# Performance work log

Hardware: AMD Instinct MI355X
Metric: run time of the kernel (lower is better)

The kernel has to match this reference:

```python
import jax, jax.numpy as jnp
import numpy as np

B, C, D, H, W = 8, 256, 128, 64, 64  # batch, in_channels, inter_dim, spatial
BN_EPS = 1e-5


def setup_inputs() -> dict:
    key = jax.random.key(0)
    ks = jax.random.split(key, 6)
    s_c = 1.0 / np.sqrt(C)
    s_d = 1.0 / np.sqrt(D)
    return {
        "x": jax.random.normal(ks[0], (B, C, H, W), dtype=jnp.float32),
        # 1x1 conv kernels, stored as [out_ch, in_ch]
        "theta_w": jax.random.normal(ks[1], (D, C), dtype=jnp.float32) * s_c,
        "phi_w": jax.random.normal(ks[2], (D, C), dtype=jnp.float32) * s_c,
        "g_w": jax.random.normal(ks[3], (D, C), dtype=jnp.float32) * s_c,
        "w_w": jax.random.normal(ks[4], (C, D), dtype=jnp.float32) * s_d,
        "w_b": jnp.zeros((C,), dtype=jnp.float32),
        "bn_gamma": jnp.ones((C,), dtype=jnp.float32),
        "bn_beta": jnp.zeros((C,), dtype=jnp.float32),
    }


def reference(x, theta_w, phi_w, g_w, w_w, w_b, bn_gamma, bn_beta):
    Bs, Cs, Hs, Ws = x.shape
    N = Hs * Ws
    xf = x.reshape(Bs, Cs, N)  # flatten spatial -> [B, C, N]

    # 1x1 convs (bias=False) == per-position channel matmuls
    theta = jnp.einsum('dc,bcn->bnd', theta_w, xf)  # [B, N, D]
    phi = jnp.einsum('dc,bcn->bdn', phi_w, xf)      # [B, D, N]
    g = jnp.einsum('dc,bcn->bnd', g_w, xf)          # [B, N, D]

    # embedded-Gaussian attention: softmax(theta @ phi) @ g
    f = jnp.einsum('bnd,bdm->bnm', theta, phi)      # [B, N, N]
    f_div_C = jax.nn.softmax(f, axis=-1)
    y = jnp.einsum('bnm,bmd->bnd', f_div_C, g)      # [B, N, D]

    # output projection W (1x1 conv with bias)
    w_y = jnp.einsum('cd,bnd->bcn', w_w, y) + w_b[None, :, None]  # [B, C, N]

    # BatchNorm (training mode: batch statistics, biased variance)
    mean = w_y.mean(axis=(0, 2))
    var = jnp.mean(jnp.square(w_y - mean[None, :, None]), axis=(0, 2))
    scale = (bn_gamma * jax.lax.rsqrt(var + BN_EPS))[None, :, None]
    w_y = (w_y - mean[None, :, None]) * scale + bn_beta[None, :, None]

    z = w_y + xf  # residual
    return z.reshape(Bs, Cs, Hs, Ws)
```

## Files before the change

### kernel.cpp

```cpp
#include <hip/hip_runtime.h>

#define BB 8
#define CC 256
#define DD 128
#define NN 4096
#define BN_EPS 1e-5f

typedef _Float16 f16;
typedef _Float16 half8 __attribute__((ext_vector_type(8)));
typedef _Float16 half2t __attribute__((ext_vector_type(2)));
typedef float f32x4 __attribute__((ext_vector_type(4)));

__device__ __forceinline__ f32x4 mfma16(half8 a, half8 b, f32x4 c) {
  return __builtin_amdgcn_mfma_f32_16x16x32_f16(a, b, c, 0, 0, 0);
}

__device__ __forceinline__ void gload_lds16(const void* g, void* l) {
  __builtin_amdgcn_global_load_lds((const __attribute__((address_space(1))) void*)g,
                                   (__attribute__((address_space(3))) void*)l, 16, 0, 0);
}

__device__ __forceinline__ half2t pkrtz(float a, float b) {
  auto t = __builtin_amdgcn_cvt_pkrtz(a, b);
  return __builtin_bit_cast(half2t, t);
}

#define EXP2(x) __builtin_amdgcn_exp2f(x)

#define PERM32(i) ((((i) >> 2) & 3) * 8 + (((i) >> 4) & 1) * 4 + ((i) & 3))

__global__ void k_cast_weights(const float* __restrict__ tw, const float* __restrict__ pw,
                               const float* __restrict__ gw, const float* __restrict__ ww,
                               f16* __restrict__ Wcat, f16* __restrict__ Wwh,
                               float* __restrict__ stats) {
  int i = blockIdx.x * 256 + threadIdx.x;
  if (i < 32768) Wcat[i] = (f16)tw[i];
  else if (i < 65536) Wcat[i] = (f16)pw[i - 32768];
  else if (i < 98304) Wcat[i] = (f16)gw[i - 65536];
  else if (i < 131072) Wwh[i - 98304] = (f16)ww[i - 98304];
  if (i < 512) stats[i] = 0.f;
}

__global__ __launch_bounds__(256) void k_gemm1(const float* __restrict__ x, const f16* __restrict__ Wcat,
                                               f16* __restrict__ T, f16* __restrict__ P,
                                               f16* __restrict__ Gdn) {
  __shared__ char xls[32768];
  __shared__ char gls[16384];
  int b = blockIdx.y;
  int n0 = blockIdx.x * 64;
  int tid = threadIdx.x;
  int lane = tid & 63, wave = tid >> 6;
  int lr = lane & 15, lg = lane >> 4;
  int wr = wave >> 1, wc = wave & 1;

  {
    int c = tid;
    const float* src = x + ((size_t)b * CC + c) * NN + n0;
#pragma unroll
    for (int n4 = 0; n4 < 64; n4 += 4) {
      f32x4 v = *(const f32x4*)(src + n4);
#pragma unroll
      for (int k = 0; k < 4; ++k) {
        int n = n4 + k;
        *(f16*)(xls + n * 512 + ((((c >> 3) ^ (n & 7)) * 8 + (c & 7)) * 2)) = (f16)v[k];
      }
    }
  }
  __syncthreads();

  half8 a[2][8];
#pragma unroll
  for (int i = 0; i < 2; ++i) {
    int nloc = wr * 32 + i * 16 + lr;
#pragma unroll
    for (int k0 = 0; k0 < 8; ++k0)
      a[i][k0] = *(const half8*)(xls + nloc * 512 + (((k0 * 4 + lg) ^ (nloc & 7)) << 4));
  }

  size_t base = (size_t)b * NN + n0;
#pragma unroll
  for (int yb = 0; yb < 6; ++yb) {
    int c0 = yb * 64 + wc * 32;
    f32x4 acc[2][2] = {};
#pragma unroll
    for (int k0 = 0; k0 < 8; ++k0) {
      half8 w[2];
      for (int j = 0; j < 2; ++j)
        w[j] = *(const half8*)(Wcat + (size_t)(c0 + j * 16 + lr) * CC + k0 * 32 + lg * 8);
      for (int i = 0; i < 2; ++i)
        for (int j = 0; j < 2; ++j)
          acc[i][j] = mfma16(a[i][k0], w[j], acc[i][j]);
    }
    if (yb < 4) {
      f16* dst = (yb < 2) ? T : P;
      int cl0 = (yb & 1) * 64 + wc * 32;
      for (int i = 0; i < 2; ++i)
        for (int j = 0; j < 2; ++j)
          for (int r = 0; r < 4; ++r) {
            int row = wr * 32 + i * 16 + lg * 4 + r;
            int col = cl0 + j * 16 + lr;
            dst[(base + row) * DD + col] = (f16)acc[i][j][r];
          }
    } else {
      for (int i = 0; i < 2; ++i)
        for (int j = 0; j < 2; ++j)
          for (int r = 0; r < 4; ++r) {
            int n = wr * 32 + i * 16 + lg * 4 + r;
            int d = (yb - 4) * 64 + wc * 32 + j * 16 + lr;
            *(f16*)(gls + n * 256 + ((((d >> 3) ^ (n & 7)) * 8 + (d & 7)) * 2)) = (f16)acc[i][j][r];
          }
    }
  }
  __syncthreads();
  {
    int d = tid >> 1, nh = (tid & 1) * 32;
    f16 tmp[32];
#pragma unroll
    for (int k = 0; k < 32; ++k) {
      int n = nh + k;
      tmp[k] = *(const f16*)(gls + n * 256 + ((((d >> 3) ^ (n & 7)) * 8 + (d & 7)) * 2));
    }
    f16* dst = Gdn + ((size_t)b * DD + d) * NN + n0 + nh;
#pragma unroll
    for (int k = 0; k < 4; ++k)
      *(half8*)(dst + k * 8) = *(const half8*)(tmp + k * 8);
  }
}

__global__ __launch_bounds__(256, 3) void k_flash(const f16* __restrict__ T, const f16* __restrict__ P,
                                                  const f16* __restrict__ Gdn, f16* __restrict__ accs,
                                                  float* __restrict__ ml) {
  __shared__ char smem[32768];
  int bid = blockIdx.x;
  int b = bid & 7;
  int u = bid >> 3;
  int hf = u % 3;
  int qx = u / 3;
  int t0 = (hf == 2) ? 86 : hf * 43;
  int nt = (hf == 2) ? 42 : 43;
  int tid = threadIdx.x;
  int lane = tid & 63, wave = tid >> 6;
  int lr = lane & 15, lg = lane >> 4;
  int q0 = qx * 128 + wave * 32;
  const f16* Tb = T + (size_t)b * NN * DD;
  const f16* Pb = P + ((size_t)b * NN + t0 * 32) * DD;
  const f16* Vb = Gdn + (size_t)b * DD * NN + t0 * 32;
  int srcq = 4 * lg;

  const f16* kbase[2];
  const f16* vbase[2];
  char* kdst[2];
  char* vdst[2];
#pragma unroll
  for (int inst = 0; inst < 2; ++inst) {
    int t = inst * 256 + tid;
    int row = t >> 4, sp = t & 15, sl = sp ^ (row & 7);
    kbase[inst] = Pb + (size_t)PERM32(row) * DD + sl * 8;
    kdst[inst] = smem + (inst * 256 + wave * 64) * 16;
    int dv = t >> 2, gv = t & 3, glv = gv ^ ((dv >> 1) & 3);
    vbase[inst] = Vb + (size_t)dv * NN + glv * 8;
    vdst[inst] = smem + 16384 + (inst * 256 + wave * 64) * 16;
  }

  half8 qf[2][4];
  for (int qt = 0; qt < 2; ++qt)
    for (int ks = 0; ks < 4; ++ks) {
      half8 v = *(const half8*)(Tb + (size_t)(q0 + qt * 16 + lr) * DD + ks * 32 + lg * 8);
      for (int j = 0; j < 8; ++j) v[j] *= (f16)1.44269504f;
      qf[qt][ks] = v;
    }
  half8 ones;
  for (int j = 0; j < 8; ++j) ones[j] = (f16)1.f;

  f32x4 acc[2][8] = {};
  f32x4 lsum[2] = {};
  float m_run[2] = {-1e30f, -1e30f};

#pragma unroll
  for (int inst = 0; inst < 2; ++inst) gload_lds16(kbase[inst], kdst[inst]);
#pragma unroll
  for (int inst = 0; inst < 2; ++inst) gload_lds16(vbase[inst], vdst[inst]);

  for (int kb = 0; kb < nt; ++kb) {
    int keyn = (kb < nt - 1) ? kb * 32 + 32 : 0;
    int cur = (kb & 1) * 8192, nxt = ((kb + 1) & 1) * 8192;
    char* Kc = smem + cur;
    char* Vc = smem + 16384 + cur;

    size_t ko = (size_t)keyn * DD;
#pragma unroll
    for (int inst = 0; inst < 2; ++inst) gload_lds16(kbase[inst] + ko, kdst[inst] + nxt);
    asm volatile("s_waitcnt vmcnt(4)" ::: "memory");
    __builtin_amdgcn_sched_barrier(0);
    __builtin_amdgcn_s_barrier();
    __builtin_amdgcn_sched_barrier(0);

    f32x4 s[2][2];
    __builtin_amdgcn_s_setprio(1);
    for (int kt = 0; kt < 2; ++kt) {
      half8 kf[4];
      for (int ks = 0; ks < 4; ++ks)
        kf[ks] = *(const half8*)(Kc + (kt * 16 + lr) * 256 + (((ks * 4 + lg) ^ (lr & 7)) << 4));
      for (int qt = 0; qt < 2; ++qt) {
        f32x4 t = {};
        for (int ks = 0; ks < 4; ++ks) t = mfma16(kf[ks], qf[qt][ks], t);
        s[qt][kt] = t;
      }
    }
    __builtin_amdgcn_s_setprio(0);

    half8 af[2];
    for (int qt = 0; qt < 2; ++qt) {
      float mx = fmaxf(fmaxf(s[qt][0][0], s[qt][0][1]), fmaxf(s[qt][0][2], s[qt][0][3]));
      mx = fmaxf(mx, fmaxf(fmaxf(s[qt][1][0], s[qt][1][1]), fmaxf(s[qt][1][2], s[qt][1][3])));
      mx = fmaxf(mx, __shfl_xor(mx, 16));
      mx = fmaxf(mx, __shfl_xor(mx, 32));
      bool grow = mx > m_run[qt] + 11.5f;
      if (__ballot(grow)) {
        float mn = fmaxf(m_run[qt], mx);
        float corr = EXP2(m_run[qt] - mn);
        m_run[qt] = mn;
        float c0 = __shfl(corr, srcq + 0), c1 = __shfl(corr, srcq + 1);
        float c2 = __shfl(corr, srcq + 2), c3 = __shfl(corr, srcq + 3);
        lsum[qt][0] *= c0; lsum[qt][1] *= c1; lsum[qt][2] *= c2; lsum[qt][3] *= c3;
        for (int nb = 0; nb < 8; ++nb) {
          acc[qt][nb][0] *= c0; acc[qt][nb][1] *= c1;
          acc[qt][nb][2] *= c2; acc[qt][nb][3] *= c3;
        }
      }
      for (int kt = 0; kt < 2; ++kt)
        for (int r = 0; r < 4; ++r)
          s[qt][kt][r] = EXP2(s[qt][kt][r] - m_run[qt]);
      union { half8 h8; half2t h2[4]; } un;
      un.h2[0] = pkrtz(s[qt][0][0], s[qt][0][1]);
      un.h2[1] = pkrtz(s[qt][0][2], s[qt][0][3]);
      un.h2[2] = pkrtz(s[qt][1][0], s[qt][1][1]);
      un.h2[3] = pkrtz(s[qt][1][2], s[qt][1][3]);
      af[qt] = un.h8;
      lsum[qt] = mfma16(af[qt], ones, lsum[qt]);
    }

#pragma unroll
    for (int inst = 0; inst < 2; ++inst) gload_lds16(vbase[inst] + keyn, vdst[inst] + nxt);
    asm volatile("s_waitcnt vmcnt(4)" ::: "memory");
    __builtin_amdgcn_sched_barrier(0);
    __builtin_amdgcn_s_barrier();
    __builtin_amdgcn_sched_barrier(0);

    __builtin_amdgcn_s_setprio(1);
    for (int nb = 0; nb < 8; ++nb) {
      int d = nb * 16 + lr;
      half8 vf = *(const half8*)(Vc + d * 64 + ((lg ^ ((d >> 1) & 3)) << 4));
      acc[0][nb] = mfma16(af[0], vf, acc[0][nb]);
      acc[1][nb] = mfma16(af[1], vf, acc[1][nb]);
    }
    __builtin_amdgcn_s_setprio(0);
  }
  asm volatile("s_waitcnt vmcnt(0)" ::: "memory");

  size_t gq0 = (size_t)b * NN + q0;
  f16* A = accs + (size_t)hf * ((size_t)BB * NN * DD) + gq0 * DD;
  for (int qt = 0; qt < 2; ++qt)
    for (int nb = 0; nb < 8; ++nb)
      for (int r = 0; r < 4; ++r)
        A[(size_t)(qt * 16 + lg * 4 + r) * DD + nb * 16 + lr] = (f16)acc[qt][nb][r];
  float* mArr = ml + hf * 32768;
  float* lArr = ml + 98304 + hf * 32768;
  if (lg == 0) {
    mArr[gq0 + lr] = m_run[0];
    mArr[gq0 + 16 + lr] = m_run[1];
  }
  if (lr == 0)
    for (int r = 0; r < 4; ++r) {
      lArr[gq0 + lg * 4 + r] = lsum[0][r];
      lArr[gq0 + 16 + lg * 4 + r] = lsum[1][r];
    }
}

__global__ __launch_bounds__(256) void k_gemm2(const f16* __restrict__ Y, const float* __restrict__ ml,
                                               const f16* __restrict__ Wwh, const float* __restrict__ wb,
                                               f16* __restrict__ wy, float* __restrict__ stats) {
  __shared__ float part[2][8][64];
  const size_t SEG = (size_t)BB * NN * DD;
  int lane = threadIdx.x & 63, wave = threadIdx.x >> 6;
  int lr = lane & 15, lg = lane >> 4;
  int wr = wave >> 1, wc = wave & 1;
  int c0 = blockIdx.y * 64 + wc * 32;
  half8 w[4][2];
  for (int k0 = 0; k0 < 4; ++k0)
    for (int j = 0; j < 2; ++j)
      w[k0][j] = *(const half8*)(Wwh + (size_t)(c0 + j * 16 + lr) * DD + k0 * 32 + lg * 8);
  float bias[2];
  for (int j = 0; j < 2; ++j) bias[j] = wb[c0 + j * 16 + lr];
  float ps[2][2] = {};
  for (int mt = 0; mt < 8; ++mt) {
    int m0 = (blockIdx.x * 8 + mt) * 64 + wr * 32;
    f16 ch[2][3];
    for (int i = 0; i < 2; ++i) {
      int row = m0 + i * 16 + lr;
      float mA = ml[row], mB = ml[32768 + row], mC = ml[65536 + row];
      float lA = ml[98304 + row], lB = ml[131072 + row], lC = ml[163840 + row];
      float mm = fmaxf(fmaxf(mA, mB), mC);
      float cA = EXP2(mA - mm), cB = EXP2(mB - mm), cC = EXP2(mC - mm);
      float inv = 1.f / (lA * cA + lB * cB + lC * cC);
      ch[i][0] = (f16)(cA * inv);
      ch[i][1] = (f16)(cB * inv);
      ch[i][2] = (f16)(cC * inv);
    }
    f32x4 acc[2][2] = {};
    for (int k0 = 0; k0 < 4; ++k0) {
      half8 a[2];
      for (int i = 0; i < 2; ++i) {
        size_t off = (size_t)(m0 + i * 16 + lr) * DD + k0 * 32 + lg * 8;
        half8 v0 = *(const half8*)(Y + off);
        half8 v1 = *(const half8*)(Y + SEG + off);
        half8 v2 = *(const half8*)(Y + 2 * SEG + off);
        a[i] = v0 * ch[i][0] + v1 * ch[i][1] + v2 * ch[i][2];
      }
      for (int i = 0; i < 2; ++i)
        for (int j = 0; j < 2; ++j)
          acc[i][j] = mfma16(a[i], w[k0][j], acc[i][j]);
    }
    for (int i = 0; i < 2; ++i)
      for (int j = 0; j < 2; ++j)
        for (int r = 0; r < 4; ++r) {
          int row = m0 + i * 16 + lg * 4 + r;
          int col = c0 + j * 16 + lr;
          float v = acc[i][j][r] + bias[j];
          wy[(size_t)row * CC + col] = (f16)v;
          ps[j][0] += v;
          ps[j][1] += v * v;
        }
  }
  for (int j = 0; j < 2; ++j) {
    int colL = wc * 32 + j * 16 + lr;
    part[0][wr * 4 + lg][colL] = ps[j][0];
    part[1][wr * 4 + lg][colL] = ps[j][1];
  }
  __syncthreads();
  if (threadIdx.x < 128) {
    int metric = threadIdx.x >> 6, col = threadIdx.x & 63;
    float s = 0.f;
    for (int wtr = 0; wtr < 8; ++wtr) s += part[metric][wtr][col];
    atomicAdd(&stats[metric * CC + blockIdx.y * 64 + col], s);
  }
}

__global__ void k_bn_apply(const f16* __restrict__ wy, const float* __restrict__ x,
                           const float* __restrict__ stats, const float* __restrict__ gamma,
                           const float* __restrict__ beta, float* __restrict__ out) {
  __shared__ f16 tile[32][33];
  int b = blockIdx.z, c0 = blockIdx.y * 32, n0 = blockIdx.x * 32;
  int tx = threadIdx.x, ty = threadIdx.y;
  for (int j = 0; j < 4; ++j) {
    int nn = ty + j * 8;
    tile[nn][tx] = wy[((size_t)b * NN + n0 + nn) * CC + c0 + tx];
  }
  __syncthreads();
  const float inv_cnt = 1.f / (float)(BB * NN);
  for (int j = 0; j < 4; ++j) {
    int cc = ty + j * 8;
    int c = c0 + cc;
    float mean = stats[c] * inv_cnt;
    float var = stats[CC + c] * inv_cnt - mean * mean;
    float scale = gamma[c] * rsqrtf(var + BN_EPS);
    size_t oi = ((size_t)b * CC + c) * NN + n0 + tx;
    out[oi] = ((float)tile[tx][cc] - mean) * scale + beta[c] + x[oi];
  }
}

extern "C" void kernel_launch(void* const* d_in, const int* in_sizes, int n_in,
                              void* d_out, int out_size, void* d_ws, size_t ws_size,
                              hipStream_t stream) {
  const float* x = (const float*)d_in[0];
  const float* tw = (const float*)d_in[1];
  const float* pw = (const float*)d_in[2];
  const float* gw = (const float*)d_in[3];
  const float* ww = (const float*)d_in[4];
  const float* wb = (const float*)d_in[5];
  const float* gamma = (const float*)d_in[6];
  const float* beta = (const float*)d_in[7];
  float* out = (float*)d_out;
  char* ws = (char*)d_ws;

  f16* Wcat = (f16*)(ws + 0);
  f16* Wwh = (f16*)(ws + 196608);
  float* stats = (float*)(ws + 262144);
  float* ml = (float*)(ws + 524288);
  const size_t BASE = 1 << 22;
  f16* T = (f16*)(ws + BASE);
  f16* P = (f16*)(ws + BASE + 8388608);
  f16* Gdn = (f16*)(ws + BASE + 16777216);
  f16* accs = (f16*)(ws + BASE + 25165824);
  f16* wy = (f16*)(ws + BASE);

  k_cast_weights<<<512, 256, 0, stream>>>(tw, pw, gw, ww, Wcat, Wwh, stats);
  k_gemm1<<<dim3(NN / 64, BB), 256, 0, stream>>>(x, Wcat, T, P, Gdn);
  k_flash<<<768, 256, 0, stream>>>(T, P, Gdn, accs, ml);
  k_gemm2<<<dim3(BB * NN / 512, CC / 64), 256, 0, stream>>>(accs, ml, Wwh, wb, wy, stats);
  k_bn_apply<<<dim3(NN / 32, CC / 32, BB), dim3(32, 8), 0, stream>>>(wy, x, stats, gamma, beta, out);
}
```

Measured before the change: 174.4 us.

## Compute all output channels per block in gemm2 to reuse merged Y tiles

k_gemm2 previously launched one block per 64-channel slice, so each block re-read and re-merged the three flash partial outputs (plus the m/l softmax stats) four times. Now each block loads and merges the Y rows once, keeps them in registers, and loops over all four 64-channel slices. The W weights are reloaded from global/L2 inside the loop. The grid drops from 256 blocks to 64, which may leave much of the GPU idle and raises register pressure.

```diff
diff --git a/kernel.cpp b/kernel.cpp
--- a/kernel.cpp
+++ b/kernel.cpp
@@ -280,19 +280,12 @@
 __global__ __launch_bounds__(256) void k_gemm2(const f16* __restrict__ Y, const float* __restrict__ ml,
                                                const f16* __restrict__ Wwh, const float* __restrict__ wb,
                                                f16* __restrict__ wy, float* __restrict__ stats) {
-  __shared__ float part[2][8][64];
+  __shared__ float part[2][8][256];
   const size_t SEG = (size_t)BB * NN * DD;
   int lane = threadIdx.x & 63, wave = threadIdx.x >> 6;
   int lr = lane & 15, lg = lane >> 4;
   int wr = wave >> 1, wc = wave & 1;
-  int c0 = blockIdx.y * 64 + wc * 32;
-  half8 w[4][2];
-  for (int k0 = 0; k0 < 4; ++k0)
-    for (int j = 0; j < 2; ++j)
-      w[k0][j] = *(const half8*)(Wwh + (size_t)(c0 + j * 16 + lr) * DD + k0 * 32 + lg * 8);
-  float bias[2];
-  for (int j = 0; j < 2; ++j) bias[j] = wb[c0 + j * 16 + lr];
-  float ps[2][2] = {};
+  float ps[4][2][2] = {};
   for (int mt = 0; mt < 8; ++mt) {
     int m0 = (blockIdx.x * 8 + mt) * 64 + wr * 32;
     f16 ch[2][3];
@@ -307,42 +300,54 @@
       ch[i][1] = (f16)(cB * inv);
       ch[i][2] = (f16)(cC * inv);
     }
-    f32x4 acc[2][2] = {};
-    for (int k0 = 0; k0 < 4; ++k0) {
-      half8 a[2];
-      for (int i = 0; i < 2; ++i) {
+    half8 a[2][4];
+    for (int i = 0; i < 2; ++i)
+      for (int k0 = 0; k0 < 4; ++k0) {
         size_t off = (size_t)(m0 + i * 16 + lr) * DD + k0 * 32 + lg * 8;
         half8 v0 = *(const half8*)(Y + off);
         half8 v1 = *(const half8*)(Y + SEG + off);
         half8 v2 = *(const half8*)(Y + 2 * SEG + off);
-        a[i] = v0 * ch[i][0] + v1 * ch[i][1] + v2 * ch[i][2];
+        a[i][k0] = v0 * ch[i][0] + v1 * ch[i][1] + v2 * ch[i][2];
+      }
+    for (int yb = 0; yb < 4; ++yb) {
+      int c0 = yb * 64 + wc * 32;
+      f32x4 acc[2][2] = {};
+      for (int k0 = 0; k0 < 4; ++k0) {
+        half8 w[2];
+        for (int j = 0; j < 2; ++j)
+          w[j] = *(const half8*)(Wwh + (size_t)(c0 + j * 16 + lr) * DD + k0 * 32 + lg * 8);
+        for (int i = 0; i < 2; ++i)
+          for (int j = 0; j < 2; ++j)
+            acc[i][j] = mfma16(a[i][k0], w[j], acc[i][j]);
       }
       for (int i = 0; i < 2; ++i)
-        for (int j = 0; j < 2; ++j)
-          acc[i][j] = mfma16(a[i], w[k0][j], acc[i][j]);
-    }
-    for (int i = 0; i < 2; ++i)
-      for (int j = 0; j < 2; ++j)
-        for (int r = 0; r < 4; ++r) {
-          int row = m0 + i * 16 + lg * 4 + r;
-          int col = c0 + j * 16 + lr;
-          float v = acc[i][j][r] + bias[j];
-          wy[(size_t)row * CC + col] = (f16)v;
-          ps[j][0] += v;
-          ps[j][1] += v * v;
+        for (int j = 0; j < 2; ++j) {
+          float bias = wb[c0 + j * 16 + lr];
+          for (int r = 0; r < 4; ++r) {
+            int row = m0 + i * 16 + lg * 4 + r;
+            int col = c0 + j * 16 + lr;
+            float v = acc[i][j][r] + bias;
+            wy[(size_t)row * CC + col] = (f16)v;
+            ps[yb][j][0] += v;
+            ps[yb][j][1] += v * v;
+          }
         }
-  }
-  for (int j = 0; j < 2; ++j) {
-    int colL = wc * 32 + j * 16 + lr;
-    part[0][wr * 4 + lg][colL] = ps[j][0];
-    part[1][wr * 4 + lg][colL] = ps[j][1];
-  }
+    }
+  }
+  for (int yb = 0; yb < 4; ++yb)
+    for (int j = 0; j < 2; ++j) {
+      int col = yb * 64 + wc * 32 + j * 16 + lr;
+      part[0][wr * 4 + lg][col] = ps[yb][j][0];
+      part[1][wr * 4 + lg][col] = ps[yb][j][1];
+    }
   __syncthreads();
-  if (threadIdx.x < 128) {
-    int metric = threadIdx.x >> 6, col = threadIdx.x & 63;
-    float s = 0.f;
-    for (int wtr = 0; wtr < 8; ++wtr) s += part[metric][wtr][col];
-    atomicAdd(&stats[metric * CC + blockIdx.y * 64 + col], s);
+  {
+    int col = threadIdx.x;
+    for (int metric = 0; metric < 2; ++metric) {
+      float s = 0.f;
+      for (int wtr = 0; wtr < 8; ++wtr) s += part[metric][wtr][col];
+      atomicAdd(&stats[metric * CC + col], s);
+    }
   }
 }
 
@@ -397,6 +402,6 @@
   k_cast_weights<<<512, 256, 0, stream>>>(tw, pw, gw, ww, Wcat, Wwh, stats);
   k_gemm1<<<dim3(NN / 64, BB), 256, 0, stream>>>(x, Wcat, T, P, Gdn);
   k_flash<<<768, 256, 0, stream>>>(T, P, Gdn, accs, ml);
-  k_gemm2<<<dim3(BB * NN / 512, CC / 64), 256, 0, stream>>>(accs, ml, Wwh, wb, wy, stats);
+  k_gemm2<<<64, 256, 0, stream>>>(accs, ml, Wwh, wb, wy, stats);
   k_bn_apply<<<dim3(NN / 32, CC / 32, BB), dim3(32, 8), 0, stream>>>(wy, x, stats, gamma, beta, out);
 }
```

Result: slower. 177.9 us (+2.0%).
